# Optimization experiments

Measured on AMD Instinct MI355X. Metric: run time of the kernel, lower is better.

Reference implementation:

```python
import jax, jax.numpy as jnp
import numpy as np


def setup_inputs() -> dict:
    key = jax.random.key(0)
    kh, ks, kwi, kwo, kcw = jax.random.split(key, 5)
    B = 2048        # decode batch (one token per request)
    H = 2048        # hidden_size
    K = 4           # conv kernel; L_cache = K - 1 = 3
    P = 8192        # req_to_token_pool size
    hidden_states = jax.random.normal(kh, (B, H), dtype=jnp.float32)
    conv_state = jax.random.normal(ks, (P, H, K - 1), dtype=jnp.float32)
    # unique, in-range pool slots (index_copy_ semantics need uniqueness)
    req_pool_indices = jnp.arange(B, dtype=jnp.int32)
    w_in = jax.random.normal(kwi, (3 * H, H), dtype=jnp.float32) * 0.02
    w_out = jax.random.normal(kwo, (H, H), dtype=jnp.float32) * 0.02
    conv_w = jax.random.normal(kcw, (H, K), dtype=jnp.float32) * 0.2
    return {
        "hidden_states": hidden_states,
        "conv_state": conv_state,
        "req_pool_indices": req_pool_indices,
        "w_in": w_in,
        "w_out": w_out,
        "conv_w": conv_w,
    }


def reference(hidden_states, conv_state, req_pool_indices, w_in, w_out, conv_w):
    """Lfm2ShortConv._forward_decode (conv_bias=False).

    Returns (y, new_conv_state) where new_conv_state is the scattered cache.
    """
    idx = req_pool_indices.astype(jnp.int32)
    # in_proj: [B, H] @ [H, 3H] -> [B, 3H]
    proj = hidden_states @ w_in.T
    B_gate, C_gate, x = jnp.split(proj, 3, axis=-1)
    Bx = B_gate * x                                  # [B, H]
    cur = conv_state[idx]                            # gather: [B, H, K-1]
    # sliding window: [old state (K-1 taps), newest token] -> [B, H, K]
    conv_in = jnp.concatenate([cur, Bx[:, :, None]], axis=-1)
    # depthwise causal conv as mul-sum over taps
    conv_out = jnp.einsum("bhk,hk->bh", conv_in, conv_w)
    y = (C_gate * conv_out) @ w_out.T                # [B, H]
    # scatter updated window (drop oldest tap)
    new_conv_state = conv_state.at[idx].set(conv_in[:, :, 1:])
    return y, new_conv_state
```

## Files before the change

kernel.cpp:

```cpp
#include <hip/hip_runtime.h>
#include <hip/hip_bf16.h>


typedef __bf16 bf16x8 __attribute__((ext_vector_type(8)));
typedef float f32x4 __attribute__((ext_vector_type(4)));

__device__ __forceinline__ unsigned short f2bf(float f) {
    union { float f; unsigned int u; } c; c.f = f;
    unsigned int u = c.u;
    u = u + 0x7FFFu + ((u >> 16) & 1u);
    return (unsigned short)(u >> 16);
}

__global__ void cvt_f32_bf16(const float4* __restrict__ src,
                             ushort4* __restrict__ dst, int n4) {
    int i = blockIdx.x * blockDim.x + threadIdx.x;
    if (i >= n4) return;
    float4 v = src[i];
    ushort4 o;
    o.x = f2bf(v.x); o.y = f2bf(v.y); o.z = f2bf(v.z); o.w = f2bf(v.w);
    dst[i] = o;
}


#define GTILE 128
#define GBK 32

__device__ __forceinline__ void gl_lds16(const unsigned short* g, unsigned short* l) {
    __builtin_amdgcn_global_load_lds(
        (const __attribute__((address_space(1))) unsigned int*)g,
        (__attribute__((address_space(3))) unsigned int*)l,
        16, 0, 0);
}

__global__ __launch_bounds__(256) void gemm_bt(
    const unsigned short* __restrict__ A,
    const unsigned short* __restrict__ B,
    float* __restrict__ C,
    int M, int N, int K)
{
    __shared__ __align__(16) unsigned short Asm[GTILE * GBK];
    __shared__ __align__(16) unsigned short Bsm[GTILE * GBK];

    const int tid  = threadIdx.x;
    const int lane = tid & 63;
    const int wave = tid >> 6;
    const int quad = lane >> 4;
    const int l16  = lane & 15;

    const int bm = blockIdx.y * GTILE;
    const int bn = blockIdx.x * GTILE;

    const int wm = (wave >> 1) * 64;
    const int wn = (wave & 1) * 64;

    f32x4 acc[4][4] = {};

    const int r0 = tid >> 2;
    const int c0 = (tid & 3) * 8;
    const unsigned short* Ag0 = A + (size_t)(bm + r0) * K + c0;
    const unsigned short* Ag1 = A + (size_t)(bm + 64 + r0) * K + c0;
    const unsigned short* Bg0 = B + (size_t)(bn + r0) * K + c0;
    const unsigned short* Bg1 = B + (size_t)(bn + 64 + r0) * K + c0;

    unsigned short* AsmW0 = Asm + wave * 512;
    unsigned short* AsmW1 = Asm + 2048 + wave * 512;
    unsigned short* BsmW0 = Bsm + wave * 512;
    unsigned short* BsmW1 = Bsm + 2048 + wave * 512;

    for (int kt = 0; kt < K; kt += GBK) {
        __syncthreads();
        gl_lds16(Ag0 + kt, AsmW0);
        gl_lds16(Ag1 + kt, AsmW1);
        gl_lds16(Bg0 + kt, BsmW0);
        gl_lds16(Bg1 + kt, BsmW1);
        __syncthreads();

        bf16x8 a[4], b[4];
#pragma unroll
        for (int i = 0; i < 4; i++)
            a[i] = *(const bf16x8*)&Asm[(wm + i * 16 + l16) * GBK + quad * 8];
#pragma unroll
        for (int j = 0; j < 4; j++)
            b[j] = *(const bf16x8*)&Bsm[(wn + j * 16 + l16) * GBK + quad * 8];
#pragma unroll
        for (int i = 0; i < 4; i++)
#pragma unroll
            for (int j = 0; j < 4; j++)
                acc[i][j] = __builtin_amdgcn_mfma_f32_16x16x32_bf16(
                    a[i], b[j], acc[i][j], 0, 0, 0);
    }

#pragma unroll
    for (int i = 0; i < 4; i++) {
#pragma unroll
        for (int j = 0; j < 4; j++) {
#pragma unroll
            for (int r = 0; r < 4; r++) {
                int row = bm + wm + i * 16 + quad * 4 + r;
                int col = bn + wn + j * 16 + l16;
                C[(size_t)row * N + col] = acc[i][j][r];
            }
        }
    }
}

__global__ void elemwise(const float* __restrict__ proj,
                         const float* __restrict__ cs_in,
                         const int* __restrict__ idx,
                         const float* __restrict__ conv_w,
                         float* __restrict__ cs_out,
                         unsigned short* __restrict__ g_bf,
                         int B, int H, int hshift, int hmask)
{
    int t = blockIdx.x * blockDim.x + threadIdx.x;
    if (t >= B * H) return;
    int b = t >> hshift;
    int h = t & hmask;
    int slot = idx[b];
    size_t prow = (size_t)b * 3 * H;
    float Bg = proj[prow + h];
    float Cg = proj[prow + H + h];
    float xv = proj[prow + 2 * H + h];
    float bx = Bg * xv;
    const float* cs = cs_in + ((size_t)slot * H + h) * 3;
    float c0 = cs[0], c1 = cs[1], c2 = cs[2];
    float4 cw = *(const float4*)(conv_w + 4 * h);
    float co = c0 * cw.x + c1 * cw.y + c2 * cw.z + bx * cw.w;
    float* os = cs_out + ((size_t)slot * H + h) * 3;
    os[0] = c1; os[1] = c2; os[2] = bx;
    g_bf[t] = f2bf(Cg * co);
}

extern "C" void kernel_launch(void* const* d_in, const int* in_sizes, int n_in,
                              void* d_out, int out_size, void* d_ws, size_t ws_size,
                              hipStream_t stream) {
    const float* hs         = (const float*)d_in[0];
    const float* conv_state = (const float*)d_in[1];
    const int*   idx        = (const int*)d_in[2];
    const float* w_in       = (const float*)d_in[3];
    const float* w_out      = (const float*)d_in[4];
    const float* conv_w     = (const float*)d_in[5];

    const int B  = in_sizes[2];
    const int H  = in_sizes[0] / B;
    const int Kc = in_sizes[5] / H;
    const int Lc = Kc - 1;
    const long long P = (long long)in_sizes[1] / ((long long)H * Lc);

    float* y_out     = (float*)d_out;
    float* state_out = y_out + (size_t)B * H;

    unsigned short* hs_bf    = (unsigned short*)d_ws;
    unsigned short* w_in_bf  = hs_bf + (size_t)B * H;
    unsigned short* w_out_bf = w_in_bf + (size_t)3 * H * H;
    float*          proj     = (float*)(w_out_bf + (size_t)H * H);
    unsigned short* g_bf     = (unsigned short*)(proj + (size_t)B * 3 * H);

    const int thr = 256;

    hipMemcpyAsync(state_out, conv_state, (size_t)P * H * Lc * sizeof(float),
                   hipMemcpyDeviceToDevice, stream);

    {
        int n4 = B * H / 4;
        cvt_f32_bf16<<<(n4 + thr - 1) / thr, thr, 0, stream>>>(
            (const float4*)hs, (ushort4*)hs_bf, n4);
    }
    {
        int n4 = 3 * H * H / 4;
        cvt_f32_bf16<<<(n4 + thr - 1) / thr, thr, 0, stream>>>(
            (const float4*)w_in, (ushort4*)w_in_bf, n4);
    }
    {
        int n4 = H * H / 4;
        cvt_f32_bf16<<<(n4 + thr - 1) / thr, thr, 0, stream>>>(
            (const float4*)w_out, (ushort4*)w_out_bf, n4);
    }

    {
        dim3 grid(3 * H / GTILE, B / GTILE);
        gemm_bt<<<grid, 256, 0, stream>>>(hs_bf, w_in_bf, proj, B, 3 * H, H);
    }

    {
        int hshift = 0; while ((1 << hshift) < H) hshift++;
        int n = B * H;
        elemwise<<<(n + thr - 1) / thr, thr, 0, stream>>>(
            proj, conv_state, idx, conv_w, state_out, g_bf, B, H, hshift, H - 1);
    }

    {
        dim3 grid(H / GTILE, B / GTILE);
        gemm_bt<<<grid, 256, 0, stream>>>(g_bf, w_out_bf, y_out, B, H, H);
    }
}
```

Baseline: 553.2 us.

## Fuse conversions, bf16 proj output, single-pass state writeback, split-K out GEMM

Merges the three f32-to-bf16 conversion launches into one prep kernel that also resets an inverse slot map. The first GEMM now writes its projection in bf16, which halves that intermediate's traffic at the cost of extra rounding. The full-pool memcpy followed by a strided scatter is replaced by a per-slot writeback kernel that either copies or shifts and appends in one pass, using the inverse index map. The output GEMM is split along K into two partial buffers, combined by a reduce kernel, to raise block count for the small 16x16 grid.

```diff
diff --git a/kernel.cpp b/kernel.cpp
--- a/kernel.cpp
+++ b/kernel.cpp
@@ -11,15 +11,32 @@
     u = u + 0x7FFFu + ((u >> 16) & 1u);
     return (unsigned short)(u >> 16);
 }
-
-__global__ void cvt_f32_bf16(const float4* __restrict__ src,
-                             ushort4* __restrict__ dst, int n4) {
+__device__ __forceinline__ float bf2f(unsigned short u) {
+    union { unsigned int i; float f; } c; c.i = ((unsigned int)u) << 16;
+    return c.f;
+}
+
+__global__ void prep(const float4* __restrict__ hs, const float4* __restrict__ wi,
+                     const float4* __restrict__ wo,
+                     ushort4* __restrict__ hs_bf, ushort4* __restrict__ wi_bf,
+                     ushort4* __restrict__ wo_bf,
+                     int* __restrict__ inv, int P,
+                     int n1, int n2, int n3) {
     int i = blockIdx.x * blockDim.x + threadIdx.x;
-    if (i >= n4) return;
-    float4 v = src[i];
-    ushort4 o;
-    o.x = f2bf(v.x); o.y = f2bf(v.y); o.z = f2bf(v.z); o.w = f2bf(v.w);
-    dst[i] = o;
+    if (i < P) inv[i] = -1;
+    const float4* s; ushort4* d; int j = i;
+    if (j < n1)            { s = hs; d = hs_bf; }
+    else if ((j -= n1) < n2) { s = wi; d = wi_bf; }
+    else if ((j -= n2) < n3) { s = wo; d = wo_bf; }
+    else return;
+    float4 v = s[j];
+    ushort4 o; o.x = f2bf(v.x); o.y = f2bf(v.y); o.z = f2bf(v.z); o.w = f2bf(v.w);
+    d[j] = o;
+}
+
+__global__ void scatter_inv(const int* __restrict__ idx, int* __restrict__ inv, int B) {
+    int b = blockIdx.x * blockDim.x + threadIdx.x;
+    if (b < B) inv[idx[b]] = b;
 }
 
 
@@ -33,11 +50,12 @@
         16, 0, 0);
 }
 
+template<int OUTBF16>
 __global__ __launch_bounds__(256) void gemm_bt(
     const unsigned short* __restrict__ A,
     const unsigned short* __restrict__ B,
-    float* __restrict__ C,
-    int M, int N, int K)
+    void* __restrict__ Cv,
+    int M, int N, int K, int ksplit)
 {
     __shared__ __align__(16) unsigned short Asm[GTILE * GBK];
     __shared__ __align__(16) unsigned short Bsm[GTILE * GBK];
@@ -50,6 +68,7 @@
 
     const int bm = blockIdx.y * GTILE;
     const int bn = blockIdx.x * GTILE;
+    const int kb = blockIdx.z * ksplit;
 
     const int wm = (wave >> 1) * 64;
     const int wn = (wave & 1) * 64;
@@ -68,7 +87,7 @@
     unsigned short* BsmW0 = Bsm + wave * 512;
     unsigned short* BsmW1 = Bsm + 2048 + wave * 512;
 
-    for (int kt = 0; kt < K; kt += GBK) {
+    for (int kt = kb; kt < kb + ksplit; kt += GBK) {
         __syncthreads();
         gl_lds16(Ag0 + kt, AsmW0);
         gl_lds16(Ag1 + kt, AsmW1);
@@ -99,17 +118,22 @@
             for (int r = 0; r < 4; r++) {
                 int row = bm + wm + i * 16 + quad * 4 + r;
                 int col = bn + wn + j * 16 + l16;
-                C[(size_t)row * N + col] = acc[i][j][r];
+                if (OUTBF16) {
+                    ((unsigned short*)Cv)[(size_t)row * N + col] = f2bf(acc[i][j][r]);
+                } else {
+                    float* Cp = (float*)Cv + (size_t)blockIdx.z * M * N;
+                    Cp[(size_t)row * N + col] = acc[i][j][r];
+                }
             }
         }
     }
 }
 
-__global__ void elemwise(const float* __restrict__ proj,
+__global__ void elemwise(const unsigned short* __restrict__ proj,
                          const float* __restrict__ cs_in,
                          const int* __restrict__ idx,
                          const float* __restrict__ conv_w,
-                         float* __restrict__ cs_out,
+                         float* __restrict__ bx_out,
                          unsigned short* __restrict__ g_bf,
                          int B, int H, int hshift, int hmask)
 {
@@ -119,17 +143,57 @@
     int h = t & hmask;
     int slot = idx[b];
     size_t prow = (size_t)b * 3 * H;
-    float Bg = proj[prow + h];
-    float Cg = proj[prow + H + h];
-    float xv = proj[prow + 2 * H + h];
+    float Bg = bf2f(proj[prow + h]);
+    float Cg = bf2f(proj[prow + H + h]);
+    float xv = bf2f(proj[prow + 2 * H + h]);
     float bx = Bg * xv;
     const float* cs = cs_in + ((size_t)slot * H + h) * 3;
     float c0 = cs[0], c1 = cs[1], c2 = cs[2];
     float4 cw = *(const float4*)(conv_w + 4 * h);
     float co = c0 * cw.x + c1 * cw.y + c2 * cw.z + bx * cw.w;
-    float* os = cs_out + ((size_t)slot * H + h) * 3;
-    os[0] = c1; os[1] = c2; os[2] = bx;
+    bx_out[t] = bx;
     g_bf[t] = f2bf(Cg * co);
+}
+
+__global__ __launch_bounds__(256) void writeback(
+    const float* __restrict__ cs_in,
+    const float* __restrict__ bx,
+    const int* __restrict__ inv,
+    float* __restrict__ cs_out,
+    int HL, int H)
+{
+    int p = blockIdx.x;
+    const float* src = cs_in + (size_t)p * HL;
+    float* dst = cs_out + (size_t)p * HL;
+    int b = inv[p];
+    int n4 = HL / 4;
+    if (b < 0) {
+        const float4* s4 = (const float4*)src;
+        float4* d4 = (float4*)dst;
+        for (int f = threadIdx.x; f < n4; f += blockDim.x) d4[f] = s4[f];
+    } else {
+        const float* bxr = bx + (size_t)b * H;
+        for (int f = threadIdx.x; f < n4; f += blockDim.x) {
+            int e0 = 4 * f;
+            float4 o;
+#pragma unroll
+            for (int j = 0; j < 4; j++) {
+                int e = e0 + j;
+                int q = e / 3, m = e - q * 3;
+                ((float*)&o)[j] = (m == 2) ? bxr[q] : src[e + 1];
+            }
+            ((float4*)dst)[f] = o;
+        }
+    }
+}
+
+__global__ void reduce2(const float4* __restrict__ p0, const float4* __restrict__ p1,
+                        float4* __restrict__ y, int n4) {
+    int i = blockIdx.x * blockDim.x + threadIdx.x;
+    if (i >= n4) return;
+    float4 a = p0[i], b = p1[i];
+    float4 o; o.x = a.x + b.x; o.y = a.y + b.y; o.z = a.z + b.z; o.w = a.w + b.w;
+    y[i] = o;
 }
 
 extern "C" void kernel_launch(void* const* d_in, const int* in_sizes, int n_in,
@@ -146,7 +210,7 @@
     const int H  = in_sizes[0] / B;
     const int Kc = in_sizes[5] / H;
     const int Lc = Kc - 1;
-    const long long P = (long long)in_sizes[1] / ((long long)H * Lc);
+    const int P  = (int)((long long)in_sizes[1] / ((long long)H * Lc));
 
     float* y_out     = (float*)d_out;
     float* state_out = y_out + (size_t)B * H;
@@ -154,44 +218,44 @@
     unsigned short* hs_bf    = (unsigned short*)d_ws;
     unsigned short* w_in_bf  = hs_bf + (size_t)B * H;
     unsigned short* w_out_bf = w_in_bf + (size_t)3 * H * H;
-    float*          proj     = (float*)(w_out_bf + (size_t)H * H);
-    unsigned short* g_bf     = (unsigned short*)(proj + (size_t)B * 3 * H);
+    unsigned short* proj_bf  = w_out_bf + (size_t)H * H;
+    unsigned short* g_bf     = proj_bf + (size_t)B * 3 * H;
+    float*          bx       = (float*)(g_bf + (size_t)B * H);
+    float*          part     = bx + (size_t)B * H;
+    int*            inv      = (int*)(part + (size_t)2 * B * H);
 
     const int thr = 256;
 
-    hipMemcpyAsync(state_out, conv_state, (size_t)P * H * Lc * sizeof(float),
-                   hipMemcpyDeviceToDevice, stream);
-
-    {
-        int n4 = B * H / 4;
-        cvt_f32_bf16<<<(n4 + thr - 1) / thr, thr, 0, stream>>>(
-            (const float4*)hs, (ushort4*)hs_bf, n4);
-    }
-    {
-        int n4 = 3 * H * H / 4;
-        cvt_f32_bf16<<<(n4 + thr - 1) / thr, thr, 0, stream>>>(
-            (const float4*)w_in, (ushort4*)w_in_bf, n4);
-    }
-    {
-        int n4 = H * H / 4;
-        cvt_f32_bf16<<<(n4 + thr - 1) / thr, thr, 0, stream>>>(
-            (const float4*)w_out, (ushort4*)w_out_bf, n4);
-    }
-
-    {
-        dim3 grid(3 * H / GTILE, B / GTILE);
-        gemm_bt<<<grid, 256, 0, stream>>>(hs_bf, w_in_bf, proj, B, 3 * H, H);
+    {
+        int n1 = B * H / 4, n2 = 3 * H * H / 4, n3 = H * H / 4;
+        int tot = n1 + n2 + n3;
+        prep<<<(tot + thr - 1) / thr, thr, 0, stream>>>(
+            (const float4*)hs, (const float4*)w_in, (const float4*)w_out,
+            (ushort4*)hs_bf, (ushort4*)w_in_bf, (ushort4*)w_out_bf,
+            inv, P, n1, n2, n3);
+    }
+    scatter_inv<<<(B + thr - 1) / thr, thr, 0, stream>>>(idx, inv, B);
+
+    {
+        dim3 grid(3 * H / GTILE, B / GTILE, 1);
+        gemm_bt<1><<<grid, 256, 0, stream>>>(hs_bf, w_in_bf, proj_bf, B, 3 * H, H, H);
     }
 
     {
         int hshift = 0; while ((1 << hshift) < H) hshift++;
         int n = B * H;
         elemwise<<<(n + thr - 1) / thr, thr, 0, stream>>>(
-            proj, conv_state, idx, conv_w, state_out, g_bf, B, H, hshift, H - 1);
-    }
-
-    {
-        dim3 grid(H / GTILE, B / GTILE);
-        gemm_bt<<<grid, 256, 0, stream>>>(g_bf, w_out_bf, y_out, B, H, H);
-    }
-}
+            proj_bf, conv_state, idx, conv_w, bx, g_bf, B, H, hshift, H - 1);
+    }
+
+    writeback<<<P, 256, 0, stream>>>(conv_state, bx, inv, state_out, 3 * H, H);
+
+    {
+        dim3 grid(H / GTILE, B / GTILE, 2);
+        gemm_bt<0><<<grid, 256, 0, stream>>>(g_bf, w_out_bf, part, B, H, H, H / 2);
+        int n4 = B * H / 4;
+        reduce2<<<(n4 + thr - 1) / thr, thr, 0, stream>>>(
+            (const float4*)part, (const float4*)(part + (size_t)B * H),
+            (float4*)y_out, n4);
+    }
+}
```

Result: faster. 534.8 us (-3.3%).
